# Kernel optimization log

Measured on AMD Instinct MI355X. Metric: run time of the kernel, lower is better.

## Reference

```python
import jax, jax.numpy as jnp
import numpy as np

EPS = 1e-5

def conv3d(x, w, b):
    y = jax.lax.conv_general_dilated(x, w, (1, 1, 1), [(1, 1), (1, 1), (1, 1)],
                                     dimension_numbers=('NCDHW', 'OIDHW', 'NCDHW'))
    return y + b[None, :, None, None, None]

def batchnorm(x, g, b):
    # training-mode BN: biased batch statistics over (N, D, H, W)
    m = jnp.mean(x, axis=(0, 2, 3, 4), keepdims=True)
    v = jnp.mean((x - m) ** 2, axis=(0, 2, 3, 4), keepdims=True)
    return (x - m) * jax.lax.rsqrt(v + EPS) * g[None, :, None, None, None] + b[None, :, None, None, None]

def deform_conv3d(x, offset, w, b):
    # x: (B,C,D,H,W); offset: (B, 3*27, D,H,W); w: (O,C,3,3,3)
    B, C, D, H, W = x.shape
    N = 27
    xp = jnp.pad(x, ((0, 0), (0, 0), (1, 1), (1, 1), (1, 1)))
    Dp, Hp, Wp = D + 2, H + 2, W + 2
    off = offset.reshape(B, 3, N, D, H, W)
    kk = jnp.arange(3, dtype=x.dtype) - 1.0  # kernel taps -1,0,1
    kd, kh, kw = [a.reshape(-1) for a in jnp.meshgrid(kk, kk, kk, indexing='ij')]
    # sampling positions in padded coords: p0 (=out idx + pad) + kernel tap + learned offset
    pd = jnp.clip((jnp.arange(D, dtype=x.dtype) + 1.0)[None, None, :, None, None]
                  + kd[None, :, None, None, None] + off[:, 0], 0.0, Dp - 1)
    ph = jnp.clip((jnp.arange(H, dtype=x.dtype) + 1.0)[None, None, None, :, None]
                  + kh[None, :, None, None, None] + off[:, 1], 0.0, Hp - 1)
    pw = jnp.clip((jnp.arange(W, dtype=x.dtype) + 1.0)[None, None, None, None, :]
                  + kw[None, :, None, None, None] + off[:, 2], 0.0, Wp - 1)
    q0d = jnp.clip(jnp.floor(pd), 0, Dp - 2); td = jnp.clip(pd - q0d, 0.0, 1.0)
    q0h = jnp.clip(jnp.floor(ph), 0, Hp - 2); th = jnp.clip(ph - q0h, 0.0, 1.0)
    q0w = jnp.clip(jnp.floor(pw), 0, Wp - 2); tw = jnp.clip(pw - q0w, 0.0, 1.0)
    q0d = q0d.astype(jnp.int32); q0h = q0h.astype(jnp.int32); q0w = q0w.astype(jnp.int32)
    xf = xp.reshape(B, C, -1)
    acc = jnp.zeros((B, C, N, D, H, W), dtype=x.dtype)
    for i in (0, 1):
        for j in (0, 1):
            for k in (0, 1):
                idx = ((q0d + i) * Hp + (q0h + j)) * Wp + (q0w + k)  # (B,N,D,H,W)
                g = ((td if i else 1.0 - td) * (th if j else 1.0 - th) * (tw if k else 1.0 - tw))
                gath = jnp.take_along_axis(xf, idx.reshape(B, 1, -1), axis=2).reshape(B, C, N, D, H, W)
                acc = acc + g[:, None] * gath
    out = jnp.einsum('bcndhw,ocn->bodhw', acc, w.reshape(w.shape[0], C, N))
    return out + b[None, :, None, None, None]


def setup_inputs() -> dict:
    ks = jax.random.split(jax.random.key(0), 16)
    s = 0.05
    f32 = jnp.float32
    return {
        'x': jax.random.normal(ks[0], (4, 1, 28, 28, 8), f32),
        'c1w': jax.random.normal(ks[1], (32, 1, 3, 3, 3), f32) * s, 'c1b': jnp.zeros((32,), f32),
        'g1': jnp.ones((32,), f32), 'b1': jnp.zeros((32,), f32),
        'c2w': jax.random.normal(ks[2], (64, 32, 3, 3, 3), f32) * s, 'c2b': jnp.zeros((64,), f32),
        'g2': jnp.ones((64,), f32), 'b2': jnp.zeros((64,), f32),
        'c3w': jax.random.normal(ks[3], (128, 64, 3, 3, 3), f32) * s, 'c3b': jnp.zeros((128,), f32),
        'g3': jnp.ones((128,), f32), 'b3': jnp.zeros((128,), f32),
        'ow': jax.random.normal(ks[4], (81, 128, 3, 3, 3), f32) * s, 'ob': jnp.zeros((81,), f32),
        'dw': jax.random.normal(ks[5], (128, 128, 3, 3, 3), f32) * s, 'db': jnp.zeros((128,), f32),
        'g4': jnp.ones((128,), f32), 'b4': jnp.zeros((128,), f32),
        'fcw': jax.random.normal(ks[6], (10, 128), f32) * s, 'fcb': jnp.zeros((10,), f32),
    }


def reference(x, c1w, c1b, g1, b1, c2w, c2b, g2, b2, c3w, c3b, g3, b3,
              ow, ob, dw, db, g4, b4, fcw, fcb):
    h = batchnorm(jax.nn.relu(conv3d(x, c1w, c1b)), g1, b1)
    h = batchnorm(jax.nn.relu(conv3d(h, c2w, c2b)), g2, b2)
    h = batchnorm(jax.nn.relu(conv3d(h, c3w, c3b)), g3, b3)
    offsets = conv3d(h, ow, ob)
    h = batchnorm(jax.nn.relu(deform_conv3d(h, offsets, dw, db)), g4, b4)
    pooled = jnp.mean(h, axis=(2, 3, 4))  # avg_pool over full (28,28,d) extent
    logits = pooled @ fcw.T + fcb
    return jax.nn.log_softmax(logits, axis=1), offsets
```

## Files before the change

kernel.cpp:

```cpp
#include <hip/hip_runtime.h>
#include <math.h>

#define BB 4
#define SP 6272
#define NSP 25088
#define EPS 1e-5f

typedef unsigned short u16;
typedef __attribute__((ext_vector_type(8))) short v8s;
typedef __attribute__((ext_vector_type(4))) float v4f;

__device__ __forceinline__ u16 f2b(float f) {
    unsigned u = __float_as_uint(f);
    return (u16)((u + 0x7fffu + ((u >> 16) & 1u)) >> 16);
}
__device__ __forceinline__ float b2f(u16 s) {
    return __uint_as_float(((unsigned)s) << 16);
}
__device__ __forceinline__ float b2f_lo(unsigned x) { return __uint_as_float(x << 16); }
__device__ __forceinline__ float b2f_hi(unsigned x) { return __uint_as_float(x & 0xffff0000u); }

__global__ __launch_bounds__(256) __attribute__((amdgpu_waves_per_eu(1, 4)))
void conv1_shfl(const float* __restrict__ X, const float* __restrict__ Wt,
                const float* __restrict__ bias, u16* __restrict__ Ybf,
                float* __restrict__ s_sum, float* __restrict__ s_sq)
{
    const int OT = 16;
    __shared__ float red[4][32];
    int xblk = blockIdx.x;
    int sblk = (xblk & 7) * 13 + (xblk >> 3);
    if (sblk >= 98) return;
    int t = threadIdx.x;
    int s = sblk * 256 + t;
    int b = s / SP;
    int sp = s - b * SP;
    int d = sp / 224;
    int r = sp - d * 224;
    int h = r >> 3;
    int w = r & 7;
    int o0 = blockIdx.y * OT;

    float mdh[9]; int odh[9];
    #pragma unroll
    for (int i = 0; i < 3; i++) {
        int dd = d + i - 1;
        float md = ((unsigned)dd < 28u) ? 1.f : 0.f;
        int ddc = min(max(dd, 0), 27);
        #pragma unroll
        for (int j = 0; j < 3; j++) {
            int hh = h + j - 1;
            float mh = ((unsigned)hh < 28u) ? 1.f : 0.f;
            int hhc = min(max(hh, 0), 27);
            mdh[i * 3 + j] = md * mh;
            odh[i * 3 + j] = ddc * 224 + hhc * 8 + w;
        }
    }
    float mw0 = (w > 0) ? 1.f : 0.f;
    float mw2 = (w < 7) ? 1.f : 0.f;

    float acc[OT];
    #pragma unroll
    for (int oo = 0; oo < OT; oo++) acc[oo] = bias[o0 + oo];

    const float* xc = X + (size_t)b * SP;
    #pragma unroll
    for (int t9 = 0; t9 < 9; t9++) {
        float x0 = xc[odh[t9]];
        float m = mdh[t9];
        float xm = __shfl_up(x0, 1, 64) * (m * mw0);
        float xz = x0 * m;
        float xp = __shfl_down(x0, 1, 64) * (m * mw2);
        #pragma unroll
        for (int oo = 0; oo < OT; oo++) {
            const float* wp = Wt + (size_t)(o0 + oo) * 27 + t9 * 3;
            acc[oo] = fmaf(xm, wp[0], acc[oo]);
            acc[oo] = fmaf(xz, wp[1], acc[oo]);
            acc[oo] = fmaf(xp, wp[2], acc[oo]);
        }
    }
    float sv[OT];
    #pragma unroll
    for (int oo = 0; oo < OT; oo++) sv[oo] = fmaxf(acc[oo], 0.f);

    unsigned pk[8];
    #pragma unroll
    for (int j = 0; j < 8; j++)
        pk[j] = (unsigned)f2b(sv[2 * j]) | ((unsigned)f2b(sv[2 * j + 1]) << 16);
    u16* row = Ybf + (size_t)(b * SP + sp) * 32 + o0;
    *(uint4*)(row)     = make_uint4(pk[0], pk[1], pk[2], pk[3]);
    *(uint4*)(row + 8) = make_uint4(pk[4], pk[5], pk[6], pk[7]);

    int l = t & 63, wvv = t >> 6;
    #pragma unroll
    for (int oo = 0; oo < OT; oo++) {
        float ss = sv[oo], qv = ss * ss;
        #pragma unroll
        for (int m = 1; m < 64; m <<= 1) {
            ss += __shfl_xor(ss, m, 64);
            qv += __shfl_xor(qv, m, 64);
        }
        if (l == 0) { red[wvv][oo] = ss; red[wvv][16 + oo] = qv; }
    }
    __syncthreads();
    if (t < 32) {
        float tot = red[0][t] + red[1][t] + red[2][t] + red[3][t];
        if (t < 16) atomicAdd(&s_sum[o0 + t], tot);
        else        atomicAdd(&s_sq[o0 + t - 16], tot);
    }
}

__global__ __launch_bounds__(256) void prepack_all(const float* __restrict__ c2w,
        const float* __restrict__ c3w, const float* __restrict__ ow,
        const float* __restrict__ dw, u16* __restrict__ wpk2,
        u16* __restrict__ wpk3, u16* __restrict__ wpko, u16* __restrict__ dwa,
        float* __restrict__ ws0)
{
    int bx = blockIdx.x;
    if (bx >= 4536) {
        int i = (bx - 4536) * 256 + threadIdx.x;
        if (i < 2048) ws0[i] = 0.f;
        return;
    }
    int idx = bx * 256 + threadIdx.x;
    if (idx < 55296) {
        int t = idx / 2048, rem = idx & 2047, o = rem >> 5, c = rem & 31;
        wpk2[idx] = f2b(c2w[((size_t)o * 32 + c) * 27 + t]);
    } else if (idx < 276480) {
        int i = idx - 55296;
        int t = i / 8192, rem = i & 8191, o = rem >> 6, c = rem & 63;
        wpk3[i] = f2b(c3w[((size_t)o * 64 + c) * 27 + t]);
    } else if (idx < 718848) {
        int i = idx - 276480;
        int t = i / 16384, rem = i & 16383, o = rem >> 7, c = rem & 127;
        wpko[i] = f2b((o < 81) ? ow[((size_t)o * 128 + c) * 27 + t] : 0.f);
    } else {
        int i = idx - 718848;
        int j = i & 7, r = (i >> 3) & 15, q = (i >> 7) & 3;
        int kc = (i >> 9) & 3, ot = (i >> 11) & 7, n = i >> 14;
        int o = ot * 16 + r, c = kc * 32 + q * 8 + j;
        dwa[i] = f2b(dw[((size_t)o * 128 + c) * 27 + n]);
    }
}

template<int CIN, int OPAD, bool OFFOUT, bool BNIN>
__global__ __launch_bounds__(256) __attribute__((amdgpu_waves_per_eu(1, 4)))
void conv_mfma(const u16* __restrict__ X, const u16* __restrict__ Wpk,
               const float* __restrict__ bias, u16* __restrict__ Ybf,
               float* __restrict__ offs, float* __restrict__ s_sum,
               float* __restrict__ s_sq, const float* __restrict__ in_sum,
               const float* __restrict__ in_sq, const float* __restrict__ in_g,
               const float* __restrict__ in_b)
{
    const int HS = CIN + 8;
    __shared__ u16 xs[160 * HS];
    __shared__ float scin[BNIN ? CIN : 1], shin[BNIN ? CIN : 1];

    int tid = threadIdx.x;
    int fid = blockIdx.x;
    int g = (fid & 7) * 98 + (fid >> 3);
    int b = g / 196;
    int rem = g - b * 196;
    int d0 = (rem / 14) * 2, h0 = (rem % 14) * 2;

    if (BNIN) {
        if (tid < CIN) {
            float m = in_sum[tid] * (1.f / NSP);
            float v = in_sq[tid] * (1.f / NSP) - m * m;
            float sc = in_g[tid] * rsqrtf(v + EPS);
            scin[tid] = sc;
            shin[tid] = in_b[tid] - m * sc;
        }
        __syncthreads();
    }

    const int NCH = CIN / 8;
    for (int idx = tid; idx < 160 * NCH; idx += 256) {
        int pos = idx / NCH, ch = idx - pos * NCH;
        int dz = pos / 40, r2 = pos - dz * 40;
        int hz = r2 / 10, wz = r2 - hz * 10;
        int dd = d0 + dz - 1, hh = h0 + hz - 1, ww = wz - 1;
        uint4 val = make_uint4(0, 0, 0, 0);
        if ((unsigned)dd < 28u && (unsigned)hh < 28u && (unsigned)ww < 8u) {
            val = *(const uint4*)(X + ((size_t)(b * SP + dd * 224 + hh * 8 + ww) * CIN + ch * 8));
            if (BNIN) {
                int cb = ch * 8;
                float f0 = b2f_lo(val.x) * scin[cb]     + shin[cb];
                float f1 = b2f_hi(val.x) * scin[cb + 1] + shin[cb + 1];
                float f2 = b2f_lo(val.y) * scin[cb + 2] + shin[cb + 2];
                float f3 = b2f_hi(val.y) * scin[cb + 3] + shin[cb + 3];
                float f4 = b2f_lo(val.z) * scin[cb + 4] + shin[cb + 4];
                float f5 = b2f_hi(val.z) * scin[cb + 5] + shin[cb + 5];
                float f6 = b2f_lo(val.w) * scin[cb + 6] + shin[cb + 6];
                float f7 = b2f_hi(val.w) * scin[cb + 7] + shin[cb + 7];
                val.x = (unsigned)f2b(f0) | ((unsigned)f2b(f1) << 16);
                val.y = (unsigned)f2b(f2) | ((unsigned)f2b(f3) << 16);
                val.z = (unsigned)f2b(f4) | ((unsigned)f2b(f5) << 16);
                val.w = (unsigned)f2b(f6) | ((unsigned)f2b(f7) << 16);
            }
        }
        *(uint4*)(xs + pos * HS + ch * 8) = val;
    }
    __syncthreads();

    int l = tid & 63, wv = tid >> 6;
    int q = l >> 4, r = l & 15;
    int hl = r >> 3, wl = r & 7;

    if (OFFOUT && blockIdx.y == 1) {
        int dl = wv >> 1;
        int o = 64 + ((wv & 1) << 4) + r;
        const u16* ap = xs + ((4 + hl + 1) * 10 + wl + 1) * HS + 8 * q + dl * 40 * HS;
        const u16* wp0 = Wpk + (size_t)o * CIN + 8 * q;
        v4f acc = {0.f, 0.f, 0.f, 0.f};
        #pragma unroll
        for (int t = 0; t < 27; t++) {
            const int koff = ((t / 9) - 1) * 40 + (((t / 3) % 3) - 1) * 10 + (t % 3) - 1;
            const u16* wt = wp0 + (size_t)t * OPAD * CIN;
            #pragma unroll
            for (int c0 = 0; c0 < CIN; c0 += 32) {
                v8s a0 = *(const v8s*)(ap + koff * HS + c0);
                v8s bf = *(const v8s*)(wt + c0);
                acc = __builtin_amdgcn_mfma_f32_16x16x32_bf16(a0, bf, acc, 0, 0, 0);
            }
        }
        float bo = (o < 81) ? bias[o] : 0.f;
        #pragma unroll
        for (int rg = 0; rg < 4; rg++) {
            int rowl = q * 4 + rg;
            int sp = (d0 + dl) * 224 + (h0 + (rowl >> 3)) * 8 + (rowl & 7);
            if (o < 81) offs[((size_t)(b * 81 + o)) * SP + sp] = acc[rg] + bo;
        }
        return;
    }

    int o_base = blockIdx.y * 64 + wv * 16;
    int o = o_base + r;

    const u16* a0p = xs + ((4 + hl + 1) * 10 + wl + 1) * HS + 8 * q;
    const u16* a1p = a0p + 40 * HS;
    const u16* wp0 = Wpk + (size_t)o * CIN + 8 * q;

    v4f acc0 = {0.f, 0.f, 0.f, 0.f}, acc1 = {0.f, 0.f, 0.f, 0.f};
    #pragma unroll
    for (int t = 0; t < 27; t++) {
        const int koff = ((t / 9) - 1) * 40 + (((t / 3) % 3) - 1) * 10 + (t % 3) - 1;
        const u16* wt = wp0 + (size_t)t * OPAD * CIN;
        #pragma unroll
        for (int c0 = 0; c0 < CIN; c0 += 32) {
            v8s a0 = *(const v8s*)(a0p + koff * HS + c0);
            v8s a1 = *(const v8s*)(a1p + koff * HS + c0);
            v8s bf = *(const v8s*)(wt + c0);
            acc0 = __builtin_amdgcn_mfma_f32_16x16x32_bf16(a0, bf, acc0, 0, 0, 0);
            acc1 = __builtin_amdgcn_mfma_f32_16x16x32_bf16(a1, bf, acc1, 0, 0, 0);
        }
    }

    if (OFFOUT) {
        float bo = (o < 81) ? bias[o] : 0.f;
        #pragma unroll
        for (int s2 = 0; s2 < 2; s2++) {
            v4f A = s2 ? acc1 : acc0;
            #pragma unroll
            for (int rg = 0; rg < 4; rg++) {
                int rowl = q * 4 + rg;
                int sp = (d0 + s2) * 224 + (h0 + (rowl >> 3)) * 8 + (rowl & 7);
                if (o < 81) offs[((size_t)(b * 81 + o)) * SP + sp] = A[rg] + bo;
            }
        }
    } else {
        float bo = bias[o];
        float rs = 0.f, rq = 0.f;
        #pragma unroll
        for (int s2 = 0; s2 < 2; s2++) {
            v4f A = s2 ? acc1 : acc0;
            #pragma unroll
            for (int rg = 0; rg < 4; rg++) {
                int rowl = q * 4 + rg;
                int sp = (d0 + s2) * 224 + (h0 + (rowl >> 3)) * 8 + (rowl & 7);
                float v = fmaxf(A[rg] + bo, 0.f);
                Ybf[(size_t)(b * SP + sp) * OPAD + o] = f2b(v);
                rs += v; rq += v * v;
            }
        }
        rs += __shfl_xor(rs, 16, 64); rs += __shfl_xor(rs, 32, 64);
        rq += __shfl_xor(rq, 16, 64); rq += __shfl_xor(rq, 32, 64);
        if (l < 16) { atomicAdd(&s_sum[o_base + l], rs); atomicAdd(&s_sq[o_base + l], rq); }
    }
}

template<int C>
__global__ __launch_bounds__(256) void bn_bf(const u16* __restrict__ Y,
        const float* __restrict__ s_sum, const float* __restrict__ s_sq,
        const float* __restrict__ g, const float* __restrict__ bb,
        u16* __restrict__ Xo)
{
    __shared__ float sc_s[C], sh_s[C];
    int t = threadIdx.x;
    if (t < C) {
        float m  = s_sum[t] * (1.f / NSP);
        float v  = s_sq[t] * (1.f / NSP) - m * m;
        float sc = g[t] * rsqrtf(v + EPS);
        sc_s[t] = sc;
        sh_s[t] = bb[t] - m * sc;
    }
    __syncthreads();
    int idx = blockIdx.x * 256 + t;
    uint4 v = ((const uint4*)Y)[idx];
    int cb = (idx & (C / 8 - 1)) * 8;
    float f0 = b2f_lo(v.x) * sc_s[cb]     + sh_s[cb];
    float f1 = b2f_hi(v.x) * sc_s[cb + 1] + sh_s[cb + 1];
    float f2 = b2f_lo(v.y) * sc_s[cb + 2] + sh_s[cb + 2];
    float f3 = b2f_hi(v.y) * sc_s[cb + 3] + sh_s[cb + 3];
    float f4 = b2f_lo(v.z) * sc_s[cb + 4] + sh_s[cb + 4];
    float f5 = b2f_hi(v.z) * sc_s[cb + 5] + sh_s[cb + 5];
    float f6 = b2f_lo(v.w) * sc_s[cb + 6] + sh_s[cb + 6];
    float f7 = b2f_hi(v.w) * sc_s[cb + 7] + sh_s[cb + 7];
    uint4 pk;
    pk.x = (unsigned)f2b(f0) | ((unsigned)f2b(f1) << 16);
    pk.y = (unsigned)f2b(f2) | ((unsigned)f2b(f3) << 16);
    pk.z = (unsigned)f2b(f4) | ((unsigned)f2b(f5) << 16);
    pk.w = (unsigned)f2b(f6) | ((unsigned)f2b(f7) << 16);
    ((uint4*)Xo)[idx] = pk;
}

__global__ __launch_bounds__(256) __attribute__((amdgpu_waves_per_eu(1, 4)))
void deform_pool(const u16* __restrict__ Ht, const float* __restrict__ OFF,
                 const u16* __restrict__ Wa, const float* __restrict__ db,
                 float* __restrict__ pooledraw, float* __restrict__ sumsq4)
{
    __shared__ float offs_lds[81 * 32];
    __shared__ int ig_s[32][8][2];
    __shared__ u16 Vb[32][136];
    __shared__ float reds[128], redq[128];

    int fid = blockIdx.x;
    int xcd = fid & 7;
    int local = fid >> 3;
    if (local >= 98) return;
    int b = xcd >> 1;
    int d = (xcd & 1) * 14 + local / 7;
    int h0 = (local % 7) * 4;

    int t = threadIdx.x;
    if (t < 128) { reds[t] = 0.f; redq[t] = 0.f; }

    int gp = t >> 3, gcr = t & 7;
    int glh = gp >> 3, gw = gp & 7, gh = h0 + glh;
    int co = t & 15, pg = t >> 4;
    int l = t & 63, wv = t >> 6;
    int q = l >> 4, r = l & 15;

    v4f acc[2][2];
    acc[0][0] = (v4f){0.f,0.f,0.f,0.f}; acc[0][1] = (v4f){0.f,0.f,0.f,0.f};
    acc[1][0] = (v4f){0.f,0.f,0.f,0.f}; acc[1][1] = (v4f){0.f,0.f,0.f,0.f};

    const u16* hb = Ht + (size_t)b * SP * 128;

    for (int i = t; i < 2592; i += 256) {
        int ch = i >> 5, p = i & 31;
        offs_lds[i] = OFF[(size_t)b * 81 * SP + (size_t)ch * SP
                          + d * 224 + (h0 + (p >> 3)) * 8 + (p & 7)];
    }

    for (int n = 0; n < 27; n++) {
        __syncthreads();
        {
            int kd = n / 9 - 1, kh = (n / 3) % 3 - 1, kw = n % 3 - 1;
            float od  = offs_lds[n * 32 + gp];
            float oh  = offs_lds[(27 + n) * 32 + gp];
            float owv = offs_lds[(54 + n) * 32 + gp];
            float pd = fminf(fmaxf((float)(d + 1 + kd) + od, 0.f), 29.f);
            float ph = fminf(fmaxf((float)(gh + 1 + kh) + oh, 0.f), 29.f);
            float pw = fminf(fmaxf((float)(gw + 1 + kw) + owv, 0.f), 9.f);
            float qd = fminf(floorf(pd), 28.f);
            float qh = fminf(floorf(ph), 28.f);
            float qw = fminf(floorf(pw), 8.f);
            float td = fminf(pd - qd, 1.f);
            float th = fminf(ph - qh, 1.f);
            float tw = fminf(pw - qw, 1.f);
            int iqd = (int)qd - 1, iqh = (int)qh - 1, iqw = (int)qw - 1;
            int i = gcr >> 2, j = (gcr >> 1) & 1, k = gcr & 1;
            int du = iqd + i, hu = iqh + j, wu = iqw + k;
            bool val = (unsigned)du < 28u && (unsigned)hu < 28u && (unsigned)wu < 8u;
            float gg = (i ? td : 1.f - td) * (j ? th : 1.f - th) * (k ? tw : 1.f - tw);
            ig_s[gp][gcr][0] = val ? (du * 224 + hu * 8 + wu) : 0;
            ig_s[gp][gcr][1] = __float_as_int(val ? gg : 0.f);
        }
        __syncthreads();
        #pragma unroll
        for (int pp = 0; pp < 2; pp++) {
            int p = pg * 2 + pp;
            float va[8] = {0.f,0.f,0.f,0.f,0.f,0.f,0.f,0.f};
            #pragma unroll
            for (int cr = 0; cr < 8; cr++) {
                int2 pr = *(const int2*)&ig_s[p][cr][0];
                float gg = __int_as_float(pr.y);
                uint4 xv = *(const uint4*)(hb + (size_t)pr.x * 128 + co * 8);
                va[0] = fmaf(gg, b2f_lo(xv.x), va[0]);
                va[1] = fmaf(gg, b2f_hi(xv.x), va[1]);
                va[2] = fmaf(gg, b2f_lo(xv.y), va[2]);
                va[3] = fmaf(gg, b2f_hi(xv.y), va[3]);
                va[4] = fmaf(gg, b2f_lo(xv.z), va[4]);
                va[5] = fmaf(gg, b2f_hi(xv.z), va[5]);
                va[6] = fmaf(gg, b2f_lo(xv.w), va[6]);
                va[7] = fmaf(gg, b2f_hi(xv.w), va[7]);
            }
            uint4 pk;
            pk.x = (unsigned)f2b(va[0]) | ((unsigned)f2b(va[1]) << 16);
            pk.y = (unsigned)f2b(va[2]) | ((unsigned)f2b(va[3]) << 16);
            pk.z = (unsigned)f2b(va[4]) | ((unsigned)f2b(va[5]) << 16);
            pk.w = (unsigned)f2b(va[6]) | ((unsigned)f2b(va[7]) << 16);
            *(uint4*)&Vb[p][co * 8] = pk;
        }
        __syncthreads();
        const u16* wn = Wa + (size_t)n * 16384;
        #pragma unroll
        for (int oti = 0; oti < 2; oti++) {
            int ot = wv * 2 + oti;
            #pragma unroll
            for (int kc = 0; kc < 4; kc++) {
                v8s af = *(const v8s*)(wn + ((((ot * 4 + kc) * 4 + q) * 16 + r) * 8));
                v8s bf0 = *(const v8s*)&Vb[r][kc * 32 + q * 8];
                v8s bf1 = *(const v8s*)&Vb[16 + r][kc * 32 + q * 8];
                acc[oti][0] = __builtin_amdgcn_mfma_f32_16x16x32_bf16(af, bf0, acc[oti][0], 0, 0, 0);
                acc[oti][1] = __builtin_amdgcn_mfma_f32_16x16x32_bf16(af, bf1, acc[oti][1], 0, 0, 0);
            }
        }
    }

    #pragma unroll
    for (int oti = 0; oti < 2; oti++) {
        #pragma unroll
        for (int rg = 0; rg < 4; rg++) {
            int o = (wv * 2 + oti) * 16 + q * 4 + rg;
            float bo = db[o];
            float v0 = fmaxf(acc[oti][0][rg] + bo, 0.f);
            float v1 = fmaxf(acc[oti][1][rg] + bo, 0.f);
            float s = v0 + v1, qq = v0 * v0 + v1 * v1;
            s += __shfl_xor(s, 1, 64);  qq += __shfl_xor(qq, 1, 64);
            s += __shfl_xor(s, 2, 64);  qq += __shfl_xor(qq, 2, 64);
            s += __shfl_xor(s, 4, 64);  qq += __shfl_xor(qq, 4, 64);
            s += __shfl_xor(s, 8, 64);  qq += __shfl_xor(qq, 8, 64);
            if (r == 0) { atomicAdd(&reds[o], s); atomicAdd(&redq[o], qq); }
        }
    }
    __syncthreads();
    if (t < 128) {
        atomicAdd(&pooledraw[b * 128 + t], reds[t]);
        atomicAdd(&sumsq4[t], redq[t]);
    }
}

__global__ __launch_bounds__(256) void final_head_emit(const float* __restrict__ pooledraw,
        const float* __restrict__ sumsq4, const float* __restrict__ g4,
        const float* __restrict__ b4, const float* __restrict__ fcw,
        const float* __restrict__ fcb, float* __restrict__ out)
{
    int t = threadIdx.x;
    __shared__ float pooled_s[4][128];
    __shared__ float logits[4][10];
    if (t < 128) {
        float s0 = pooledraw[t], s1 = pooledraw[128 + t];
        float s2 = pooledraw[256 + t], s3 = pooledraw[384 + t];
        float tot = s0 + s1 + s2 + s3;
        float m  = tot * (1.f / NSP);
        float v  = sumsq4[t] * (1.f / NSP) - m * m;
        float sc = g4[t] * rsqrtf(v + EPS);
        float sh = b4[t] - m * sc;
        pooled_s[0][t] = s0 * (1.f / SP) * sc + sh;
        pooled_s[1][t] = s1 * (1.f / SP) * sc + sh;
        pooled_s[2][t] = s2 * (1.f / SP) * sc + sh;
        pooled_s[3][t] = s3 * (1.f / SP) * sc + sh;
    }
    __syncthreads();
    if (t < 40) {
        int b = t / 10, j = t % 10;
        float l = fcb[j];
        for (int c = 0; c < 128; c++) l = fmaf(pooled_s[b][c], fcw[j * 128 + c], l);
        logits[b][j] = l;
    }
    __syncthreads();
    if (t < 4) {
        float mx = -1e30f;
        for (int j = 0; j < 10; j++) mx = fmaxf(mx, logits[t][j]);
        float se = 0.f;
        for (int j = 0; j < 10; j++) se += expf(logits[t][j] - mx);
        float lse = mx + logf(se);
        for (int j = 0; j < 10; j++) out[t * 10 + j] = logits[t][j] - lse;
    }
}

extern "C" void kernel_launch(void* const* d_in, const int* in_sizes, int n_in,
                              void* d_out, int out_size, void* d_ws, size_t ws_size,
                              hipStream_t stream)
{
    (void)in_sizes; (void)n_in; (void)out_size; (void)ws_size;
    const float* x   = (const float*)d_in[0];
    const float* c1w = (const float*)d_in[1];
    const float* c1b = (const float*)d_in[2];
    const float* g1  = (const float*)d_in[3];
    const float* b1  = (const float*)d_in[4];
    const float* c2w = (const float*)d_in[5];
    const float* c2b = (const float*)d_in[6];
    const float* g2  = (const float*)d_in[7];
    const float* b2  = (const float*)d_in[8];
    const float* c3w = (const float*)d_in[9];
    const float* c3b = (const float*)d_in[10];
    const float* g3  = (const float*)d_in[11];
    const float* b3  = (const float*)d_in[12];
    const float* ow  = (const float*)d_in[13];
    const float* ob  = (const float*)d_in[14];
    const float* dw  = (const float*)d_in[15];
    const float* db  = (const float*)d_in[16];
    const float* g4  = (const float*)d_in[17];
    const float* b4  = (const float*)d_in[18];
    const float* fcw = (const float*)d_in[19];
    const float* fcb = (const float*)d_in[20];

    float* ws = (float*)d_ws;
    float* S1 = ws + 0,   *Q1 = ws + 32;
    float* S2 = ws + 64,  *Q2 = ws + 128;
    float* S3 = ws + 192, *Q3 = ws + 320;
    float* PO = ws + 448;
    float* Q4 = ws + 960;
    u16* y1bf = (u16*)(ws + 2048);
    u16* y2bf = y1bf + 802816;
    u16* y3bf = y2bf + 1605632;
    u16* x3bf = y3bf + 3211264;
    u16* wpk2 = x3bf + 3211264;
    u16* wpk3 = wpk2 + 55296;
    u16* wpko = wpk3 + 221184;
    u16* dwa  = wpko + 442368;

    float* outf = (float*)d_out;
    float* offp = outf + 40;

    prepack_all<<<4544, 256, 0, stream>>>(c2w, c3w, ow, dw, wpk2, wpk3, wpko, dwa, ws);

    conv1_shfl<<<dim3(104, 2), 256, 0, stream>>>(x, c1w, c1b, y1bf, S1, Q1);

    conv_mfma<32, 64, false, true><<<dim3(784, 1), 256, 0, stream>>>(
        y1bf, wpk2, c2b, y2bf, nullptr, S2, Q2, S1, Q1, g1, b1);

    conv_mfma<64, 128, false, true><<<dim3(784, 2), 256, 0, stream>>>(
        y2bf, wpk3, c3b, y3bf, nullptr, S3, Q3, S2, Q2, g2, b2);

    bn_bf<128><<<1568, 256, 0, stream>>>(y3bf, S3, Q3, g3, b3, x3bf);

    conv_mfma<128, 128, true, false><<<dim3(784, 2), 256, 0, stream>>>(
        x3bf, wpko, ob, nullptr, offp, nullptr, nullptr, nullptr, nullptr, nullptr, nullptr);
    deform_pool<<<800, 256, 0, stream>>>(x3bf, offp, dwa, db, PO, Q4);
    final_head_emit<<<1, 256, 0, stream>>>(PO, Q4, g4, b4, fcw, fcb, outf);
}
```

Before: 417.5 us.

## Fold BN3 into deform weights and fuse head into deform kernel

Removes the standalone BN3 pass over the 128-channel activation. BN is applied on the fly inside the offset conv, and for the deform conv it is folded algebraically: weights are pre-scaled by the BN scale, and a per-tap shift term weighted by the sum of bilinear coefficients is added. Extra blocks in the offset-conv launch compute the scaled weights and shift constants. The final head kernel is merged into deform_pool through a last-block atomic counter, and bf16 packing uses the hardware conversion intrinsic. The risks are rounding differences from bf16 weight folding and a counter in the workspace that must start at zero each call.

```diff
diff --git a/kernel.cpp b/kernel.cpp
--- a/kernel.cpp
+++ b/kernel.cpp
@@ -1,4 +1,5 @@
 #include <hip/hip_runtime.h>
+#include <hip/hip_bf16.h>
 #include <math.h>
 
 #define BB 4
@@ -19,6 +20,12 @@
 }
 __device__ __forceinline__ float b2f_lo(unsigned x) { return __uint_as_float(x << 16); }
 __device__ __forceinline__ float b2f_hi(unsigned x) { return __uint_as_float(x & 0xffff0000u); }
+__device__ __forceinline__ unsigned pk2(float a, float b) {
+    __hip_bfloat162 h = __float22bfloat162_rn(make_float2(a, b));
+    unsigned u;
+    __builtin_memcpy(&u, &h, 4);
+    return u;
+}
 
 __global__ __launch_bounds__(256) __attribute__((amdgpu_waves_per_eu(1, 4)))
 void conv1_shfl(const float* __restrict__ X, const float* __restrict__ Wt,
@@ -84,8 +91,7 @@
 
     unsigned pk[8];
     #pragma unroll
-    for (int j = 0; j < 8; j++)
-        pk[j] = (unsigned)f2b(sv[2 * j]) | ((unsigned)f2b(sv[2 * j + 1]) << 16);
+    for (int j = 0; j < 8; j++) pk[j] = pk2(sv[2 * j], sv[2 * j + 1]);
     u16* row = Ybf + (size_t)(b * SP + sp) * 32 + o0;
     *(uint4*)(row)     = make_uint4(pk[0], pk[1], pk[2], pk[3]);
     *(uint4*)(row + 8) = make_uint4(pk[4], pk[5], pk[6], pk[7]);
@@ -142,14 +148,15 @@
     }
 }
 
-template<int CIN, int OPAD, bool OFFOUT, bool BNIN>
+template<int CIN, int OPAD, bool OFFOUT, bool BNIN, bool FOLD>
 __global__ __launch_bounds__(256) __attribute__((amdgpu_waves_per_eu(1, 4)))
 void conv_mfma(const u16* __restrict__ X, const u16* __restrict__ Wpk,
                const float* __restrict__ bias, u16* __restrict__ Ybf,
                float* __restrict__ offs, float* __restrict__ s_sum,
                float* __restrict__ s_sq, const float* __restrict__ in_sum,
                const float* __restrict__ in_sq, const float* __restrict__ in_g,
-               const float* __restrict__ in_b)
+               const float* __restrict__ in_b, const u16* __restrict__ dwa_in,
+               u16* __restrict__ dwa2, float* __restrict__ Kn)
 {
     const int HS = CIN + 8;
     __shared__ u16 xs[160 * HS];
@@ -171,6 +178,49 @@
             shin[tid] = in_b[tid] - m * sc;
         }
         __syncthreads();
+    }
+
+    if (FOLD && fid >= 784) {
+        int fb = fid - 784;
+        if (blockIdx.y == 0) {
+            for (int i = fb * 256 + tid; i < 55296; i += 3584) {
+                v8s wv8 = *(const v8s*)(dwa_in + (size_t)i * 8);
+                int ii = i * 8;
+                int cb = ((ii >> 9) & 3) * 32 + ((ii >> 7) & 3) * 8;
+                float f0 = b2f((u16)wv8[0]) * scin[cb + 0];
+                float f1 = b2f((u16)wv8[1]) * scin[cb + 1];
+                float f2 = b2f((u16)wv8[2]) * scin[cb + 2];
+                float f3 = b2f((u16)wv8[3]) * scin[cb + 3];
+                float f4 = b2f((u16)wv8[4]) * scin[cb + 4];
+                float f5 = b2f((u16)wv8[5]) * scin[cb + 5];
+                float f6 = b2f((u16)wv8[6]) * scin[cb + 6];
+                float f7 = b2f((u16)wv8[7]) * scin[cb + 7];
+                uint4 pk;
+                pk.x = pk2(f0, f1); pk.y = pk2(f2, f3);
+                pk.z = pk2(f4, f5); pk.w = pk2(f6, f7);
+                *(uint4*)(dwa2 + (size_t)i * 8) = pk;
+            }
+        } else {
+            int i = fb * 256 + tid;
+            if (i < 3456) {
+                int n = i >> 7, o = i & 127, ot = o >> 4, rr = o & 15;
+                float acc = 0.f;
+                #pragma unroll
+                for (int kc = 0; kc < 4; kc++) {
+                    #pragma unroll
+                    for (int qq = 0; qq < 4; qq++) {
+                        v8s wv8 = *(const v8s*)(dwa_in +
+                            (size_t)((((n * 8 + ot) * 4 + kc) * 4 + qq) * 16 + rr) * 8);
+                        int cb = kc * 32 + qq * 8;
+                        #pragma unroll
+                        for (int j = 0; j < 8; j++)
+                            acc = fmaf(b2f((u16)wv8[j]), shin[cb + j], acc);
+                    }
+                }
+                Kn[i] = acc;
+            }
+        }
+        return;
     }
 
     const int NCH = CIN / 8;
@@ -192,10 +242,8 @@
                 float f5 = b2f_hi(val.z) * scin[cb + 5] + shin[cb + 5];
                 float f6 = b2f_lo(val.w) * scin[cb + 6] + shin[cb + 6];
                 float f7 = b2f_hi(val.w) * scin[cb + 7] + shin[cb + 7];
-                val.x = (unsigned)f2b(f0) | ((unsigned)f2b(f1) << 16);
-                val.y = (unsigned)f2b(f2) | ((unsigned)f2b(f3) << 16);
-                val.z = (unsigned)f2b(f4) | ((unsigned)f2b(f5) << 16);
-                val.w = (unsigned)f2b(f6) | ((unsigned)f2b(f7) << 16);
+                val.x = pk2(f0, f1); val.y = pk2(f2, f3);
+                val.z = pk2(f4, f5); val.w = pk2(f6, f7);
             }
         }
         *(uint4*)(xs + pos * HS + ch * 8) = val;
@@ -288,205 +336,193 @@
     }
 }
 
-template<int C>
-__global__ __launch_bounds__(256) void bn_bf(const u16* __restrict__ Y,
-        const float* __restrict__ s_sum, const float* __restrict__ s_sq,
-        const float* __restrict__ g, const float* __restrict__ bb,
-        u16* __restrict__ Xo)
-{
-    __shared__ float sc_s[C], sh_s[C];
-    int t = threadIdx.x;
-    if (t < C) {
-        float m  = s_sum[t] * (1.f / NSP);
-        float v  = s_sq[t] * (1.f / NSP) - m * m;
-        float sc = g[t] * rsqrtf(v + EPS);
-        sc_s[t] = sc;
-        sh_s[t] = bb[t] - m * sc;
-    }
-    __syncthreads();
-    int idx = blockIdx.x * 256 + t;
-    uint4 v = ((const uint4*)Y)[idx];
-    int cb = (idx & (C / 8 - 1)) * 8;
-    float f0 = b2f_lo(v.x) * sc_s[cb]     + sh_s[cb];
-    float f1 = b2f_hi(v.x) * sc_s[cb + 1] + sh_s[cb + 1];
-    float f2 = b2f_lo(v.y) * sc_s[cb + 2] + sh_s[cb + 2];
-    float f3 = b2f_hi(v.y) * sc_s[cb + 3] + sh_s[cb + 3];
-    float f4 = b2f_lo(v.z) * sc_s[cb + 4] + sh_s[cb + 4];
-    float f5 = b2f_hi(v.z) * sc_s[cb + 5] + sh_s[cb + 5];
-    float f6 = b2f_lo(v.w) * sc_s[cb + 6] + sh_s[cb + 6];
-    float f7 = b2f_hi(v.w) * sc_s[cb + 7] + sh_s[cb + 7];
-    uint4 pk;
-    pk.x = (unsigned)f2b(f0) | ((unsigned)f2b(f1) << 16);
-    pk.y = (unsigned)f2b(f2) | ((unsigned)f2b(f3) << 16);
-    pk.z = (unsigned)f2b(f4) | ((unsigned)f2b(f5) << 16);
-    pk.w = (unsigned)f2b(f6) | ((unsigned)f2b(f7) << 16);
-    ((uint4*)Xo)[idx] = pk;
-}
-
 __global__ __launch_bounds__(256) __attribute__((amdgpu_waves_per_eu(1, 4)))
 void deform_pool(const u16* __restrict__ Ht, const float* __restrict__ OFF,
-                 const u16* __restrict__ Wa, const float* __restrict__ db,
-                 float* __restrict__ pooledraw, float* __restrict__ sumsq4)
+                 const u16* __restrict__ Wa, const float* __restrict__ Kn,
+                 const float* __restrict__ db, float* __restrict__ pooledraw,
+                 float* __restrict__ sumsq4, unsigned* __restrict__ cnt,
+                 const float* __restrict__ g4, const float* __restrict__ b4,
+                 const float* __restrict__ fcw, const float* __restrict__ fcb,
+                 float* __restrict__ out)
 {
     __shared__ float offs_lds[81 * 32];
     __shared__ int ig_s[32][8][2];
     __shared__ u16 Vb[32][136];
     __shared__ float reds[128], redq[128];
+    __shared__ float gs_s[32];
+    __shared__ unsigned done_s;
 
     int fid = blockIdx.x;
     int xcd = fid & 7;
     int local = fid >> 3;
-    if (local >= 98) return;
-    int b = xcd >> 1;
-    int d = (xcd & 1) * 14 + local / 7;
-    int h0 = (local % 7) * 4;
-
     int t = threadIdx.x;
-    if (t < 128) { reds[t] = 0.f; redq[t] = 0.f; }
-
-    int gp = t >> 3, gcr = t & 7;
-    int glh = gp >> 3, gw = gp & 7, gh = h0 + glh;
-    int co = t & 15, pg = t >> 4;
-    int l = t & 63, wv = t >> 6;
-    int q = l >> 4, r = l & 15;
-
-    v4f acc[2][2];
-    acc[0][0] = (v4f){0.f,0.f,0.f,0.f}; acc[0][1] = (v4f){0.f,0.f,0.f,0.f};
-    acc[1][0] = (v4f){0.f,0.f,0.f,0.f}; acc[1][1] = (v4f){0.f,0.f,0.f,0.f};
-
-    const u16* hb = Ht + (size_t)b * SP * 128;
-
-    for (int i = t; i < 2592; i += 256) {
-        int ch = i >> 5, p = i & 31;
-        offs_lds[i] = OFF[(size_t)b * 81 * SP + (size_t)ch * SP
-                          + d * 224 + (h0 + (p >> 3)) * 8 + (p & 7)];
-    }
-
-    for (int n = 0; n < 27; n++) {
+
+    if (local < 98) {
+        int b = xcd >> 1;
+        int d = (xcd & 1) * 14 + local / 7;
+        int h0 = (local % 7) * 4;
+
+        if (t < 128) { reds[t] = 0.f; redq[t] = 0.f; }
+
+        int gp = t >> 3, gcr = t & 7;
+        int glh = gp >> 3, gw = gp & 7, gh = h0 + glh;
+        int co = t & 15, pg = t >> 4;
+        int l = t & 63, wv = t >> 6;
+        int q = l >> 4, r = l & 15;
+
+        v4f acc[2][2];
+        acc[0][0] = (v4f){0.f,0.f,0.f,0.f}; acc[0][1] = (v4f){0.f,0.f,0.f,0.f};
+        acc[1][0] = (v4f){0.f,0.f,0.f,0.f}; acc[1][1] = (v4f){0.f,0.f,0.f,0.f};
+
+        const u16* hb = Ht + (size_t)b * SP * 128;
+
+        for (int i = t; i < 2592; i += 256) {
+            int ch = i >> 5, p = i & 31;
+            offs_lds[i] = OFF[(size_t)b * 81 * SP + (size_t)ch * SP
+                              + d * 224 + (h0 + (p >> 3)) * 8 + (p & 7)];
+        }
+
+        for (int n = 0; n < 27; n++) {
+            __syncthreads();
+            {
+                int kd = n / 9 - 1, kh = (n / 3) % 3 - 1, kw = n % 3 - 1;
+                float od  = offs_lds[n * 32 + gp];
+                float oh  = offs_lds[(27 + n) * 32 + gp];
+                float owv = offs_lds[(54 + n) * 32 + gp];
+                float pd = fminf(fmaxf((float)(d + 1 + kd) + od, 0.f), 29.f);
+                float ph = fminf(fmaxf((float)(gh + 1 + kh) + oh, 0.f), 29.f);
+                float pw = fminf(fmaxf((float)(gw + 1 + kw) + owv, 0.f), 9.f);
+                float qd = fminf(floorf(pd), 28.f);
+                float qh = fminf(floorf(ph), 28.f);
+                float qw = fminf(floorf(pw), 8.f);
+                float td = fminf(pd - qd, 1.f);
+                float th = fminf(ph - qh, 1.f);
+                float tw = fminf(pw - qw, 1.f);
+                int iqd = (int)qd - 1, iqh = (int)qh - 1, iqw = (int)qw - 1;
+                int i = gcr >> 2, j = (gcr >> 1) & 1, k = gcr & 1;
+                int du = iqd + i, hu = iqh + j, wu = iqw + k;
+                bool val = (unsigned)du < 28u && (unsigned)hu < 28u && (unsigned)wu < 8u;
+                float gg = (i ? td : 1.f - td) * (j ? th : 1.f - th) * (k ? tw : 1.f - tw);
+                float ggm = val ? gg : 0.f;
+                ig_s[gp][gcr][0] = val ? (du * 224 + hu * 8 + wu) : 0;
+                ig_s[gp][gcr][1] = __float_as_int(ggm);
+                float gsum = ggm;
+                gsum += __shfl_xor(gsum, 1, 64);
+                gsum += __shfl_xor(gsum, 2, 64);
+                gsum += __shfl_xor(gsum, 4, 64);
+                if (gcr == 0) gs_s[gp] = gsum;
+            }
+            __syncthreads();
+            #pragma unroll
+            for (int pp = 0; pp < 2; pp++) {
+                int p = pg * 2 + pp;
+                float va[8] = {0.f,0.f,0.f,0.f,0.f,0.f,0.f,0.f};
+                #pragma unroll
+                for (int cr = 0; cr < 8; cr++) {
+                    int2 pr = *(const int2*)&ig_s[p][cr][0];
+                    float gg = __int_as_float(pr.y);
+                    uint4 xv = *(const uint4*)(hb + (size_t)pr.x * 128 + co * 8);
+                    va[0] = fmaf(gg, b2f_lo(xv.x), va[0]);
+                    va[1] = fmaf(gg, b2f_hi(xv.x), va[1]);
+                    va[2] = fmaf(gg, b2f_lo(xv.y), va[2]);
+                    va[3] = fmaf(gg, b2f_hi(xv.y), va[3]);
+                    va[4] = fmaf(gg, b2f_lo(xv.z), va[4]);
+                    va[5] = fmaf(gg, b2f_hi(xv.z), va[5]);
+                    va[6] = fmaf(gg, b2f_lo(xv.w), va[6]);
+                    va[7] = fmaf(gg, b2f_hi(xv.w), va[7]);
+                }
+                uint4 pk;
+                pk.x = pk2(va[0], va[1]); pk.y = pk2(va[2], va[3]);
+                pk.z = pk2(va[4], va[5]); pk.w = pk2(va[6], va[7]);
+                *(uint4*)&Vb[p][co * 8] = pk;
+            }
+            __syncthreads();
+            const u16* wn = Wa + (size_t)n * 16384;
+            #pragma unroll
+            for (int oti = 0; oti < 2; oti++) {
+                int ot = wv * 2 + oti;
+                #pragma unroll
+                for (int kc = 0; kc < 4; kc++) {
+                    v8s af = *(const v8s*)(wn + ((((ot * 4 + kc) * 4 + q) * 16 + r) * 8));
+                    v8s bf0 = *(const v8s*)&Vb[r][kc * 32 + q * 8];
+                    v8s bf1 = *(const v8s*)&Vb[16 + r][kc * 32 + q * 8];
+                    acc[oti][0] = __builtin_amdgcn_mfma_f32_16x16x32_bf16(af, bf0, acc[oti][0], 0, 0, 0);
+                    acc[oti][1] = __builtin_amdgcn_mfma_f32_16x16x32_bf16(af, bf1, acc[oti][1], 0, 0, 0);
+                }
+            }
+            {
+                float gsa = gs_s[r], gsb = gs_s[16 + r];
+                const v4f k0 = *(const v4f*)(Kn + n * 128 + wv * 32 + q * 4);
+                const v4f k1 = *(const v4f*)(Kn + n * 128 + wv * 32 + 16 + q * 4);
+                acc[0][0] += k0 * gsa; acc[0][1] += k0 * gsb;
+                acc[1][0] += k1 * gsa; acc[1][1] += k1 * gsb;
+            }
+        }
+
+        #pragma unroll
+        for (int oti = 0; oti < 2; oti++) {
+            #pragma unroll
+            for (int rg = 0; rg < 4; rg++) {
+                int o = (wv * 2 + oti) * 16 + q * 4 + rg;
+                float bo = db[o];
+                float v0 = fmaxf(acc[oti][0][rg] + bo, 0.f);
+                float v1 = fmaxf(acc[oti][1][rg] + bo, 0.f);
+                float s = v0 + v1, qq = v0 * v0 + v1 * v1;
+                s += __shfl_xor(s, 1, 64);  qq += __shfl_xor(qq, 1, 64);
+                s += __shfl_xor(s, 2, 64);  qq += __shfl_xor(qq, 2, 64);
+                s += __shfl_xor(s, 4, 64);  qq += __shfl_xor(qq, 4, 64);
+                s += __shfl_xor(s, 8, 64);  qq += __shfl_xor(qq, 8, 64);
+                if (r == 0) { atomicAdd(&reds[o], s); atomicAdd(&redq[o], qq); }
+            }
+        }
         __syncthreads();
-        {
-            int kd = n / 9 - 1, kh = (n / 3) % 3 - 1, kw = n % 3 - 1;
-            float od  = offs_lds[n * 32 + gp];
-            float oh  = offs_lds[(27 + n) * 32 + gp];
-            float owv = offs_lds[(54 + n) * 32 + gp];
-            float pd = fminf(fmaxf((float)(d + 1 + kd) + od, 0.f), 29.f);
-            float ph = fminf(fmaxf((float)(gh + 1 + kh) + oh, 0.f), 29.f);
-            float pw = fminf(fmaxf((float)(gw + 1 + kw) + owv, 0.f), 9.f);
-            float qd = fminf(floorf(pd), 28.f);
-            float qh = fminf(floorf(ph), 28.f);
-            float qw = fminf(floorf(pw), 8.f);
-            float td = fminf(pd - qd, 1.f);
-            float th = fminf(ph - qh, 1.f);
-            float tw = fminf(pw - qw, 1.f);
-            int iqd = (int)qd - 1, iqh = (int)qh - 1, iqw = (int)qw - 1;
-            int i = gcr >> 2, j = (gcr >> 1) & 1, k = gcr & 1;
-            int du = iqd + i, hu = iqh + j, wu = iqw + k;
-            bool val = (unsigned)du < 28u && (unsigned)hu < 28u && (unsigned)wu < 8u;
-            float gg = (i ? td : 1.f - td) * (j ? th : 1.f - th) * (k ? tw : 1.f - tw);
-            ig_s[gp][gcr][0] = val ? (du * 224 + hu * 8 + wu) : 0;
-            ig_s[gp][gcr][1] = __float_as_int(val ? gg : 0.f);
+        if (t < 128) {
+            atomicAdd(&pooledraw[b * 128 + t], reds[t]);
+            atomicAdd(&sumsq4[t], redq[t]);
+        }
+    }
+
+    __syncthreads();
+    if (t == 0) {
+        __threadfence();
+        done_s = atomicAdd(cnt, 1u);
+    }
+    __syncthreads();
+    if (done_s == 799u) {
+        __shared__ float pooled_s[4][128];
+        __shared__ float logits_s[4][10];
+        if (t < 128) {
+            float s0 = __hip_atomic_load(&pooledraw[t],       __ATOMIC_RELAXED, __HIP_MEMORY_SCOPE_AGENT);
+            float s1 = __hip_atomic_load(&pooledraw[128 + t], __ATOMIC_RELAXED, __HIP_MEMORY_SCOPE_AGENT);
+            float s2 = __hip_atomic_load(&pooledraw[256 + t], __ATOMIC_RELAXED, __HIP_MEMORY_SCOPE_AGENT);
+            float s3 = __hip_atomic_load(&pooledraw[384 + t], __ATOMIC_RELAXED, __HIP_MEMORY_SCOPE_AGENT);
+            float qv = __hip_atomic_load(&sumsq4[t],          __ATOMIC_RELAXED, __HIP_MEMORY_SCOPE_AGENT);
+            float tot = s0 + s1 + s2 + s3;
+            float m  = tot * (1.f / NSP);
+            float v  = qv * (1.f / NSP) - m * m;
+            float sc = g4[t] * rsqrtf(v + EPS);
+            float sh = b4[t] - m * sc;
+            pooled_s[0][t] = s0 * (1.f / SP) * sc + sh;
+            pooled_s[1][t] = s1 * (1.f / SP) * sc + sh;
+            pooled_s[2][t] = s2 * (1.f / SP) * sc + sh;
+            pooled_s[3][t] = s3 * (1.f / SP) * sc + sh;
         }
         __syncthreads();
-        #pragma unroll
-        for (int pp = 0; pp < 2; pp++) {
-            int p = pg * 2 + pp;
-            float va[8] = {0.f,0.f,0.f,0.f,0.f,0.f,0.f,0.f};
-            #pragma unroll
-            for (int cr = 0; cr < 8; cr++) {
-                int2 pr = *(const int2*)&ig_s[p][cr][0];
-                float gg = __int_as_float(pr.y);
-                uint4 xv = *(const uint4*)(hb + (size_t)pr.x * 128 + co * 8);
-                va[0] = fmaf(gg, b2f_lo(xv.x), va[0]);
-                va[1] = fmaf(gg, b2f_hi(xv.x), va[1]);
-                va[2] = fmaf(gg, b2f_lo(xv.y), va[2]);
-                va[3] = fmaf(gg, b2f_hi(xv.y), va[3]);
-                va[4] = fmaf(gg, b2f_lo(xv.z), va[4]);
-                va[5] = fmaf(gg, b2f_hi(xv.z), va[5]);
-                va[6] = fmaf(gg, b2f_lo(xv.w), va[6]);
-                va[7] = fmaf(gg, b2f_hi(xv.w), va[7]);
-            }
-            uint4 pk;
-            pk.x = (unsigned)f2b(va[0]) | ((unsigned)f2b(va[1]) << 16);
-            pk.y = (unsigned)f2b(va[2]) | ((unsigned)f2b(va[3]) << 16);
-            pk.z = (unsigned)f2b(va[4]) | ((unsigned)f2b(va[5]) << 16);
-            pk.w = (unsigned)f2b(va[6]) | ((unsigned)f2b(va[7]) << 16);
-            *(uint4*)&Vb[p][co * 8] = pk;
+        if (t < 40) {
+            int b = t / 10, j = t % 10;
+            float lg = fcb[j];
+            for (int c = 0; c < 128; c++) lg = fmaf(pooled_s[b][c], fcw[j * 128 + c], lg);
+            logits_s[b][j] = lg;
         }
         __syncthreads();
-        const u16* wn = Wa + (size_t)n * 16384;
-        #pragma unroll
-        for (int oti = 0; oti < 2; oti++) {
-            int ot = wv * 2 + oti;
-            #pragma unroll
-            for (int kc = 0; kc < 4; kc++) {
-                v8s af = *(const v8s*)(wn + ((((ot * 4 + kc) * 4 + q) * 16 + r) * 8));
-                v8s bf0 = *(const v8s*)&Vb[r][kc * 32 + q * 8];
-                v8s bf1 = *(const v8s*)&Vb[16 + r][kc * 32 + q * 8];
-                acc[oti][0] = __builtin_amdgcn_mfma_f32_16x16x32_bf16(af, bf0, acc[oti][0], 0, 0, 0);
-                acc[oti][1] = __builtin_amdgcn_mfma_f32_16x16x32_bf16(af, bf1, acc[oti][1], 0, 0, 0);
-            }
-        }
-    }
-
-    #pragma unroll
-    for (int oti = 0; oti < 2; oti++) {
-        #pragma unroll
-        for (int rg = 0; rg < 4; rg++) {
-            int o = (wv * 2 + oti) * 16 + q * 4 + rg;
-            float bo = db[o];
-            float v0 = fmaxf(acc[oti][0][rg] + bo, 0.f);
-            float v1 = fmaxf(acc[oti][1][rg] + bo, 0.f);
-            float s = v0 + v1, qq = v0 * v0 + v1 * v1;
-            s += __shfl_xor(s, 1, 64);  qq += __shfl_xor(qq, 1, 64);
-            s += __shfl_xor(s, 2, 64);  qq += __shfl_xor(qq, 2, 64);
-            s += __shfl_xor(s, 4, 64);  qq += __shfl_xor(qq, 4, 64);
-            s += __shfl_xor(s, 8, 64);  qq += __shfl_xor(qq, 8, 64);
-            if (r == 0) { atomicAdd(&reds[o], s); atomicAdd(&redq[o], qq); }
-        }
-    }
-    __syncthreads();
-    if (t < 128) {
-        atomicAdd(&pooledraw[b * 128 + t], reds[t]);
-        atomicAdd(&sumsq4[t], redq[t]);
-    }
-}
-
-__global__ __launch_bounds__(256) void final_head_emit(const float* __restrict__ pooledraw,
-        const float* __restrict__ sumsq4, const float* __restrict__ g4,
-        const float* __restrict__ b4, const float* __restrict__ fcw,
-        const float* __restrict__ fcb, float* __restrict__ out)
-{
-    int t = threadIdx.x;
-    __shared__ float pooled_s[4][128];
-    __shared__ float logits[4][10];
-    if (t < 128) {
-        float s0 = pooledraw[t], s1 = pooledraw[128 + t];
-        float s2 = pooledraw[256 + t], s3 = pooledraw[384 + t];
-        float tot = s0 + s1 + s2 + s3;
-        float m  = tot * (1.f / NSP);
-        float v  = sumsq4[t] * (1.f / NSP) - m * m;
-        float sc = g4[t] * rsqrtf(v + EPS);
-        float sh = b4[t] - m * sc;
-        pooled_s[0][t] = s0 * (1.f / SP) * sc + sh;
-        pooled_s[1][t] = s1 * (1.f / SP) * sc + sh;
-        pooled_s[2][t] = s2 * (1.f / SP) * sc + sh;
-        pooled_s[3][t] = s3 * (1.f / SP) * sc + sh;
-    }
-    __syncthreads();
-    if (t < 40) {
-        int b = t / 10, j = t % 10;
-        float l = fcb[j];
-        for (int c = 0; c < 128; c++) l = fmaf(pooled_s[b][c], fcw[j * 128 + c], l);
-        logits[b][j] = l;
-    }
-    __syncthreads();
-    if (t < 4) {
-        float mx = -1e30f;
-        for (int j = 0; j < 10; j++) mx = fmaxf(mx, logits[t][j]);
-        float se = 0.f;
-        for (int j = 0; j < 10; j++) se += expf(logits[t][j] - mx);
-        float lse = mx + logf(se);
-        for (int j = 0; j < 10; j++) out[t * 10 + j] = logits[t][j] - lse;
+        if (t < 4) {
+            float mx = -1e30f;
+            for (int j = 0; j < 10; j++) mx = fmaxf(mx, logits_s[t][j]);
+            float se = 0.f;
+            for (int j = 0; j < 10; j++) se += expf(logits_s[t][j] - mx);
+            float lse = mx + logf(se);
+            for (int j = 0; j < 10; j++) out[t * 10 + j] = logits_s[t][j] - lse;
+        }
     }
 }
 
@@ -523,14 +559,16 @@
     float* S3 = ws + 192, *Q3 = ws + 320;
     float* PO = ws + 448;
     float* Q4 = ws + 960;
+    unsigned* cnt = (unsigned*)(ws + 1100);
     u16* y1bf = (u16*)(ws + 2048);
     u16* y2bf = y1bf + 802816;
     u16* y3bf = y2bf + 1605632;
-    u16* x3bf = y3bf + 3211264;
-    u16* wpk2 = x3bf + 3211264;
+    u16* wpk2 = y3bf + 3211264;
     u16* wpk3 = wpk2 + 55296;
     u16* wpko = wpk3 + 221184;
     u16* dwa  = wpko + 442368;
+    u16* dwa2 = dwa  + 442368;
+    float* Kn = (float*)(dwa2 + 442368);
 
     float* outf = (float*)d_out;
     float* offp = outf + 40;
@@ -539,16 +577,18 @@
 
     conv1_shfl<<<dim3(104, 2), 256, 0, stream>>>(x, c1w, c1b, y1bf, S1, Q1);
 
-    conv_mfma<32, 64, false, true><<<dim3(784, 1), 256, 0, stream>>>(
-        y1bf, wpk2, c2b, y2bf, nullptr, S2, Q2, S1, Q1, g1, b1);
-
-    conv_mfma<64, 128, false, true><<<dim3(784, 2), 256, 0, stream>>>(
-        y2bf, wpk3, c3b, y3bf, nullptr, S3, Q3, S2, Q2, g2, b2);
-
-    bn_bf<128><<<1568, 256, 0, stream>>>(y3bf, S3, Q3, g3, b3, x3bf);
-
-    conv_mfma<128, 128, true, false><<<dim3(784, 2), 256, 0, stream>>>(
-        x3bf, wpko, ob, nullptr, offp, nullptr, nullptr, nullptr, nullptr, nullptr, nullptr);
-    deform_pool<<<800, 256, 0, stream>>>(x3bf, offp, dwa, db, PO, Q4);
-    final_head_emit<<<1, 256, 0, stream>>>(PO, Q4, g4, b4, fcw, fcb, outf);
-}
+    conv_mfma<32, 64, false, true, false><<<dim3(784, 1), 256, 0, stream>>>(
+        y1bf, wpk2, c2b, y2bf, nullptr, S2, Q2, S1, Q1, g1, b1,
+        nullptr, nullptr, nullptr);
+
+    conv_mfma<64, 128, false, true, false><<<dim3(784, 2), 256, 0, stream>>>(
+        y2bf, wpk3, c3b, y3bf, nullptr, S3, Q3, S2, Q2, g2, b2,
+        nullptr, nullptr, nullptr);
+
+    conv_mfma<128, 128, true, true, true><<<dim3(798, 2), 256, 0, stream>>>(
+        y3bf, wpko, ob, nullptr, offp, nullptr, nullptr, S3, Q3, g3, b3,
+        dwa, dwa2, Kn);
+
+    deform_pool<<<800, 256, 0, stream>>>(y3bf, offp, dwa2, Kn, db, PO, Q4, cnt,
+                                         g4, b4, fcw, fcb, outf);
+}
```

New measurement: 431.3 us. +3.3%, slower.
